# Performance work log

Hardware: AMD Instinct MI355X
Metric: run time of the kernel (lower is better)

## Reference

```python
import jax, jax.numpy as jnp
import numpy as np

B, H, D, DV, N, M = 1, 8, 64, 64, 2048, 128


def setup_inputs() -> dict:
    key = jax.random.key(0)
    k1, k2, k3, k4 = jax.random.split(key, 4)
    keys = jax.random.normal(k1, (B, H, D, N), dtype=jnp.float32)
    values = jax.random.normal(k2, (B, H, DV, N), dtype=jnp.float32)
    queries = jax.random.normal(k3, (B, H, D, N), dtype=jnp.float32)
    # orthonormal random features: QR of (m, key_dim) gaussian (reduced QR, m >= key_dim)
    raw = np.asarray(jax.random.normal(k4, (M, D), dtype=jnp.float32), dtype=np.float64)
    features = jnp.asarray(np.linalg.qr(raw)[0], dtype=jnp.float32)  # (M, D)
    return {"keys": keys, "values": values, "queries": queries, "features": features}


def reference(keys, values, queries, features):
    b, h, d, n = keys.shape
    dv = values.shape[2]
    m = features.shape[0]
    phi_scale = 1.0 / jnp.sqrt(jnp.asarray(m, keys.dtype))
    # flatten heads into batch, move locations to axis 1: (B*H, N, D)
    k = keys.reshape(b * h, d, n).transpose(0, 2, 1)
    v = values.reshape(b * h, dv, n).transpose(0, 2, 1)
    q = queries.reshape(b * h, d, n).transpose(0, 2, 1)

    def phi(x):  # (BH, N, D) -> (BH, N, M); f=[relu], h(x)=1.0
        return jax.nn.relu(jnp.einsum('bnd,md->bnm', x, features)) * phi_scale

    phi_k = phi(k)
    phi_q = phi(q)
    # causal linear attention: prefix sums of phi_k (x) v outer products
    kv = jnp.cumsum(phi_k[:, :, :, None] * v[:, :, None, :], axis=1)  # (BH, N, M, DV)
    out = jnp.einsum('bnm,bnmv->bnv', phi_q, kv)                      # (BH, N, DV)
    norm = jnp.einsum('bnm,bnm->bn', phi_q, jnp.cumsum(phi_k, axis=1))
    out = out / norm[:, :, None]
    out = out.transpose(0, 2, 1).reshape(b, h, dv, n)
    return out
```

## Files before the change

### kernel.cpp

```cpp
#include <hip/hip_runtime.h>


#define BH 8
#define D 64
#define DV 64
#define NSEQ 2048
#define M 128
#define CHK 64
#define NC (NSEQ / CHK)
#define PHI_SCALE 0.08838834764831845f

typedef unsigned int uint;
typedef unsigned short ushort;
typedef __attribute__((ext_vector_type(8))) short bf16x8;
typedef __attribute__((ext_vector_type(4))) float f32x4;
#define MFMA16(a, b, c) __builtin_amdgcn_mfma_f32_16x16x32_bf16((a), (b), (c), 0, 0, 0)

__device__ __forceinline__ short f2bf(float x) {
    uint u = __float_as_uint(x);
    u += 0x7fffu + ((u >> 16) & 1u);
    return (short)(u >> 16);
}
__device__ __forceinline__ float bf2f(short b) {
    return __uint_as_float(((uint)(ushort)b) << 16);
}

__global__ __launch_bounds__(256) void favor_p1(
    const float* __restrict__ keys, const float* __restrict__ values,
    const float* __restrict__ features, ushort* __restrict__ St,
    float* __restrict__ z)
{
    const int bh = blockIdx.x >> 5, c = blockIdx.x & 31, n0 = c * CHK;
    const int tid = threadIdx.x;
    const int lane = tid & 63, wid = tid >> 6, quad = lane >> 4, l16 = lane & 15;

    __shared__ ulong2 smv[2048];
    short* sF  = (short*)smv;
    short* sPK = (short*)smv + 8192;

    for (int i = tid; i < 8192; i += 256) sF[i] = f2bf(features[i]);
    __syncthreads();

    {
        const float* Kb = keys + bh * D * NSEQ + n0 + 16 * wid + l16;
        bf16x8 bK[2];
        for (int h = 0; h < 2; ++h)
            for (int j = 0; j < 8; ++j)
                bK[h][j] = f2bf(Kb[(32 * h + 8 * quad + j) * NSEQ]);
        for (int mt = 0; mt < 8; ++mt) {
            f32x4 acc = {0.f, 0.f, 0.f, 0.f};
            for (int h = 0; h < 2; ++h) {
                bf16x8 aF = *(const bf16x8*)(sF + (16 * mt + l16) * 64 + 32 * h + 8 * quad);
                acc = MFMA16(aF, bK[h], acc);
            }
            for (int r = 0; r < 4; ++r)
                sPK[(16 * mt + 4 * quad + r) * 64 + 16 * wid + l16] =
                    f2bf(fmaxf(acc[r], 0.f) * PHI_SCALE);
        }
    }
    __syncthreads();

    if (tid < 128) {
        float s = 0.f;
        for (int n = 0; n < 64; ++n) s += bf2f(sPK[tid * 64 + ((n + tid) & 63)]);
        z[(bh * NC + c) * M + tid] = s;
    }

    {
        const float* Vb = values + bh * DV * NSEQ + n0;
        bf16x8 aV[2];
        for (int h = 0; h < 2; ++h) {
            const float4* vp = (const float4*)(Vb + (16 * wid + l16) * NSEQ + 32 * h + 8 * quad);
            float4 v0 = vp[0], v1 = vp[1];
            aV[h][0] = f2bf(v0.x); aV[h][1] = f2bf(v0.y);
            aV[h][2] = f2bf(v0.z); aV[h][3] = f2bf(v0.w);
            aV[h][4] = f2bf(v1.x); aV[h][5] = f2bf(v1.y);
            aV[h][6] = f2bf(v1.z); aV[h][7] = f2bf(v1.w);
        }
        ushort* So = St + (size_t)(bh * NC + c) * (DV * M);
        for (int mt = 0; mt < 8; ++mt) {
            f32x4 acc = {0.f, 0.f, 0.f, 0.f};
            for (int h = 0; h < 2; ++h) {
                bf16x8 bP = *(const bf16x8*)(sPK + (16 * mt + l16) * 64 + 32 * h + 8 * quad);
                acc = MFMA16(aV[h], bP, acc);
            }
            for (int r = 0; r < 4; ++r)
                So[(16 * wid + 4 * quad + r) * M + 16 * mt + l16] = (ushort)f2bf(acc[r]);
        }
    }
}

__global__ __launch_bounds__(256) void favor_p2(ushort* __restrict__ St,
                                                float* __restrict__ z)
{
    const int gid = blockIdx.x * 256 + threadIdx.x;
    if (blockIdx.x < 256) {
        const int bh = gid >> 13, vm = gid & 8191;
        ushort* p = St + (size_t)bh * NC * 8192 + vm;
        float vals[NC];
        #pragma unroll
        for (int cc = 0; cc < NC; ++cc) vals[cc] = bf2f(p[cc * 8192]);
        float run = 0.f;
        #pragma unroll
        for (int cc = 0; cc < NC; ++cc) { p[cc * 8192] = (ushort)f2bf(run); run += vals[cc]; }
    } else {
        const int i = gid - 65536;
        if (i < BH * M) {
            const int bh = i >> 7, m = i & 127;
            float* p = z + bh * NC * M + m;
            float vals[NC];
            #pragma unroll
            for (int cc = 0; cc < NC; ++cc) vals[cc] = p[cc * M];
            float run = 0.f;
            #pragma unroll
            for (int cc = 0; cc < NC; ++cc) { p[cc * M] = run; run += vals[cc]; }
        }
    }
}

__global__ __launch_bounds__(256) void favor_p3(
    const float* __restrict__ keys, const float* __restrict__ values,
    const float* __restrict__ queries, const ushort* __restrict__ St,
    const float* __restrict__ z, const float* __restrict__ features,
    float* __restrict__ out)
{
    const int bh = blockIdx.x >> 5, c = blockIdx.x & 31, n0 = c * CHK;
    const int tid = threadIdx.x;
    const int lane = tid & 63, wid = tid >> 6, quad = lane >> 4, l16 = lane & 15;

    __shared__ ulong2 smv[3120];
    char* sm = (char*)smv;
    short* sF   = (short*)sm;
    short* sAm  = (short*)sm;
    short* sV   = (short*)(sm + 8192);
    short* sPQ  = (short*)(sm + 16384);
    float* sOut = (float*)(sm + 16384);
    short* sPK  = (short*)(sm + 32768);
    float* sZ   = (float*)(sm + 49152);
    float* sNm  = (float*)(sm + 49664);

    for (int i = tid; i < 8192; i += 256) sF[i] = f2bf(features[i]);
    if (tid < 128) sZ[tid] = z[(bh * NC + c) * M + tid];
    __syncthreads();

    {
        const float* Qb = queries + bh * D * NSEQ + n0 + 16 * wid + l16;
        const float* Kb = keys    + bh * D * NSEQ + n0 + 16 * wid + l16;
        bf16x8 aQ[2], aK[2];
        for (int h = 0; h < 2; ++h)
            for (int j = 0; j < 8; ++j) {
                const int d = 32 * h + 8 * quad + j;
                aQ[h][j] = f2bf(Qb[d * NSEQ]);
                aK[h][j] = f2bf(Kb[d * NSEQ]);
            }
        for (int mt = 0; mt < 8; ++mt) {
            f32x4 accQ = {0.f, 0.f, 0.f, 0.f}, accK = {0.f, 0.f, 0.f, 0.f};
            for (int h = 0; h < 2; ++h) {
                bf16x8 bF = *(const bf16x8*)(sF + (16 * mt + l16) * 64 + 32 * h + 8 * quad);
                accQ = MFMA16(aQ[h], bF, accQ);
                accK = MFMA16(aK[h], bF, accK);
            }
            for (int r = 0; r < 4; ++r) {
                const int row = (16 * wid + 4 * quad + r) * M + 16 * mt + l16;
                sPQ[row] = f2bf(fmaxf(accQ[r], 0.f) * PHI_SCALE);
                sPK[row] = f2bf(fmaxf(accK[r], 0.f) * PHI_SCALE);
            }
        }
    }
    __syncthreads();

    f32x4 accO[4], accC[4];
    for (int t = 0; t < 4; ++t) { accO[t] = (f32x4){0.f,0.f,0.f,0.f}; accC[t] = (f32x4){0.f,0.f,0.f,0.f}; }
    {
        const ushort* Sb = St + (size_t)(bh * NC + c) * (DV * M);
        for (int mt = 0; mt < 4; ++mt) {
            bf16x8 aP = *(const bf16x8*)(sPQ + (16 * wid + l16) * M + 32 * mt + 8 * quad);
            for (int vt = 0; vt < 4; ++vt) {
                bf16x8 bS = *(const bf16x8*)(Sb + (16 * vt + l16) * M + 32 * mt + 8 * quad);
                accO[vt] = MFMA16(aP, bS, accO[vt]);
            }
            for (int jt = 0; jt < 4; ++jt) {
                bf16x8 bK2 = *(const bf16x8*)(sPK + (16 * jt + l16) * M + 32 * mt + 8 * quad);
                accC[jt] = MFMA16(aP, bK2, accC[jt]);
            }
        }
    }
    float rsum[4] = {0.f, 0.f, 0.f, 0.f};
    for (int jt = 0; jt < 4; ++jt)
        for (int r = 0; r < 4; ++r) {
            const int n = 16 * wid + 4 * quad + r;
            const int j = 16 * jt + l16;
            const float av = (j <= n) ? accC[jt][r] : 0.f;
            rsum[r] += av;
            sAm[n * 64 + j] = f2bf(av);
        }
    for (int r = 0; r < 4; ++r) {
        float s = rsum[r];
        s += __shfl_xor(s, 1); s += __shfl_xor(s, 2);
        s += __shfl_xor(s, 4); s += __shfl_xor(s, 8);
        if (l16 == 0) sNm[16 * wid + 4 * quad + r] = s;
    }
    __syncthreads();

    for (int i = tid; i < 4096; i += 256) {
        const int v = i >> 6, j = i & 63;
        sV[v * 64 + j] = f2bf(values[(bh * DV + v) * NSEQ + n0 + j]);
    }
    if (tid < 64) {
        float s = 0.f;
        for (int mm = 0; mm < 128; ++mm) {
            const int m = (mm + 2 * tid) & 127;
            s += bf2f(sPQ[tid * M + m]) * sZ[m];
        }
        sNm[tid] += s;
    }
    __syncthreads();

    for (int jh = 0; jh < 2; ++jh) {
        bf16x8 aA = *(const bf16x8*)(sAm + (16 * wid + l16) * 64 + 32 * jh + 8 * quad);
        for (int vt = 0; vt < 4; ++vt) {
            bf16x8 bV = *(const bf16x8*)(sV + (16 * vt + l16) * 64 + 32 * jh + 8 * quad);
            accO[vt] = MFMA16(aA, bV, accO[vt]);
        }
    }
    for (int vt = 0; vt < 4; ++vt)
        for (int r = 0; r < 4; ++r) {
            const int n = 16 * wid + 4 * quad + r, v = 16 * vt + l16;
            sOut[n * 65 + v] = accO[vt][r] / sNm[n];
        }
    __syncthreads();

    for (int i = tid; i < 4096; i += 256) {
        const int v = i >> 6, n = i & 63;
        out[(bh * DV + v) * NSEQ + n0 + n] = sOut[n * 65 + v];
    }
}

extern "C" void kernel_launch(void* const* d_in, const int* in_sizes, int n_in,
                              void* d_out, int out_size, void* d_ws, size_t ws_size,
                              hipStream_t stream)
{
    (void)in_sizes; (void)n_in; (void)out_size; (void)ws_size;
    const float* keys     = (const float*)d_in[0];
    const float* values   = (const float*)d_in[1];
    const float* queries  = (const float*)d_in[2];
    const float* features = (const float*)d_in[3];
    float* outp = (float*)d_out;

    ushort* St = (ushort*)d_ws;
    float*  z  = (float*)((char*)d_ws + (size_t)BH * NC * DV * M * sizeof(ushort));

    favor_p1<<<dim3(BH * NC), dim3(256), 0, stream>>>(keys, values, features, St, z);
    favor_p2<<<dim3(260), dim3(256), 0, stream>>>(St, z);
    favor_p3<<<dim3(BH * NC), dim3(256), 0, stream>>>(keys, values, queries, St, z,
                                                      features, outp);
}
```

Baseline: 91.66 us.

## Restructure into four-kernel pipeline with pre-transposed bf16 inputs and smaller chunks

Adds a pre-pass kernel that converts queries, keys and features to bf16 in transposed, row-contiguous layouts. All intra-chunk work (phi_q, phi_k, chunk states, the causal intra-chunk output and its normalizer) moves into the first pass, so the final pass only applies the prefix state, adds the stored intra-chunk result and normalizes. Chunk size drops from 64 to 32, which doubles the number of blocks and halves per-block work to improve parallelism. In exchange it adds a kernel launch and extra workspace traffic for phiQ, Y and the normalizer, and doubles the state tensor and the length of the prefix scan.

```diff
diff --git a/kernel.cpp b/kernel.cpp
--- a/kernel.cpp
+++ b/kernel.cpp
@@ -2,12 +2,12 @@
 
 
 #define BH 8
-#define D 64
+#define DD 64
 #define DV 64
 #define NSEQ 2048
-#define M 128
-#define CHK 64
-#define NC (NSEQ / CHK)
+#define MM 128
+#define CK 32
+#define NCH (NSEQ / CK)
 #define PHI_SCALE 0.08838834764831845f
 
 typedef unsigned int uint;
@@ -21,73 +21,183 @@
     u += 0x7fffu + ((u >> 16) & 1u);
     return (short)(u >> 16);
 }
-__device__ __forceinline__ float bf2f(short b) {
-    return __uint_as_float(((uint)(ushort)b) << 16);
+__device__ __forceinline__ float bf2f(ushort b) {
+    return __uint_as_float(((uint)b) << 16);
+}
+
+#define OFF_QT   0u
+#define OFF_KT   2097152u
+#define OFF_FB   4194304u
+#define OFF_PQT  4210688u
+#define OFF_ST   8404992u
+#define OFF_Z    16793600u
+#define OFF_Y    17055744u
+#define OFF_NI   21250048u
+
+__global__ __launch_bounds__(256) void favor_p0(
+    const float* __restrict__ keys, const float* __restrict__ queries,
+    const float* __restrict__ features, ushort* __restrict__ Qt,
+    ushort* __restrict__ Kt, ushort* __restrict__ Fb)
+{
+    const int b = blockIdx.x, tid = threadIdx.x;
+    if (b == 256) {
+        uint* fo = (uint*)Fb;
+        const float2* fi = (const float2*)features;
+        for (int i = tid; i < 4096; i += 256) {
+            float2 f = fi[i];
+            fo[i] = (uint)(ushort)f2bf(f.x) | ((uint)(ushort)f2bf(f.y) << 16);
+        }
+        return;
+    }
+    const int bh = b >> 5, nc = b & 31, n0 = nc * 64;
+    __shared__ short sT[64 * 66];
+    for (int pass = 0; pass < 2; ++pass) {
+        const float* src = pass ? keys : queries;
+        ushort* dst = pass ? Kt : Qt;
+        for (int i = tid; i < 4096; i += 256) {
+            const int d = i >> 6, n = i & 63;
+            sT[d * 66 + n] = f2bf(src[(bh * 64 + d) * NSEQ + n0 + n]);
+        }
+        __syncthreads();
+        uint* dw = (uint*)dst;
+        for (int i = tid; i < 2048; i += 256) {
+            const int n = i >> 5, dp = i & 31;
+            const uint lo = (ushort)sT[(2 * dp) * 66 + n];
+            const uint hi = (ushort)sT[(2 * dp + 1) * 66 + n];
+            dw[(size_t)(bh * NSEQ + n0 + n) * 32 + dp] = lo | (hi << 16);
+        }
+        __syncthreads();
+    }
 }
 
 __global__ __launch_bounds__(256) void favor_p1(
-    const float* __restrict__ keys, const float* __restrict__ values,
-    const float* __restrict__ features, ushort* __restrict__ St,
-    float* __restrict__ z)
-{
-    const int bh = blockIdx.x >> 5, c = blockIdx.x & 31, n0 = c * CHK;
+    const float* __restrict__ values, const ushort* __restrict__ Qt,
+    const ushort* __restrict__ Kt, const ushort* __restrict__ Fb,
+    ushort* __restrict__ phiQT, ushort* __restrict__ St,
+    float* __restrict__ z, float* __restrict__ Yw, float* __restrict__ normI)
+{
+    const int bh = blockIdx.x >> 6, ck = blockIdx.x & 63, n0 = ck * CK;
     const int tid = threadIdx.x;
     const int lane = tid & 63, wid = tid >> 6, quad = lane >> 4, l16 = lane & 15;
 
-    __shared__ ulong2 smv[2048];
-    short* sF  = (short*)smv;
-    short* sPK = (short*)smv + 8192;
-
-    for (int i = tid; i < 8192; i += 256) sF[i] = f2bf(features[i]);
-    __syncthreads();
-
-    {
-        const float* Kb = keys + bh * D * NSEQ + n0 + 16 * wid + l16;
-        bf16x8 bK[2];
+    __shared__ __align__(16) short sPQT[32 * 136];
+    __shared__ __align__(16) short sPKT[32 * 136];
+    __shared__ __align__(16) short sPK[128 * 40];
+    __shared__ __align__(16) short sV[64 * 40];
+    __shared__ __align__(16) short sAm[32 * 40];
+    __shared__ float sNI[64];
+
+    for (int i = tid; i < 2048; i += 256) {
+        const int v = i >> 5, j = i & 31;
+        sV[v * 40 + j] = f2bf(values[(bh * DV + v) * NSEQ + n0 + j]);
+    }
+
+    {
+        const int nt = wid & 1, mg = wid >> 1;
+        const ushort* qrow = Qt + (size_t)(bh * NSEQ + n0 + 16 * nt + l16) * 64;
+        const ushort* krow = Kt + (size_t)(bh * NSEQ + n0 + 16 * nt + l16) * 64;
+        bf16x8 aQ[2], aK[2];
+        for (int h = 0; h < 2; ++h) {
+            aQ[h] = *(const bf16x8*)(qrow + 32 * h + 8 * quad);
+            aK[h] = *(const bf16x8*)(krow + 32 * h + 8 * quad);
+        }
+        for (int t = 0; t < 4; ++t) {
+            const int mt = mg * 4 + t;
+            f32x4 accQ = {0.f, 0.f, 0.f, 0.f}, accK = {0.f, 0.f, 0.f, 0.f};
+            for (int h = 0; h < 2; ++h) {
+                bf16x8 bF = *(const bf16x8*)(Fb + (16 * mt + l16) * 64 + 32 * h + 8 * quad);
+                accQ = MFMA16(aQ[h], bF, accQ);
+                accK = MFMA16(aK[h], bF, accK);
+            }
+            for (int r = 0; r < 4; ++r) {
+                const int nl = 16 * nt + 4 * quad + r, m = 16 * mt + l16;
+                sPQT[nl * 136 + m] = f2bf(fmaxf(accQ[r], 0.f) * PHI_SCALE);
+                sPKT[nl * 136 + m] = f2bf(fmaxf(accK[r], 0.f) * PHI_SCALE);
+            }
+        }
+    }
+    for (int t = 0; t < 2; ++t) {
+        const int mt = wid * 2 + t;
+        bf16x8 aF[2];
         for (int h = 0; h < 2; ++h)
-            for (int j = 0; j < 8; ++j)
-                bK[h][j] = f2bf(Kb[(32 * h + 8 * quad + j) * NSEQ]);
-        for (int mt = 0; mt < 8; ++mt) {
+            aF[h] = *(const bf16x8*)(Fb + (16 * mt + l16) * 64 + 32 * h + 8 * quad);
+        for (int ntt = 0; ntt < 2; ++ntt) {
             f32x4 acc = {0.f, 0.f, 0.f, 0.f};
             for (int h = 0; h < 2; ++h) {
-                bf16x8 aF = *(const bf16x8*)(sF + (16 * mt + l16) * 64 + 32 * h + 8 * quad);
-                acc = MFMA16(aF, bK[h], acc);
+                bf16x8 bK = *(const bf16x8*)(Kt + (size_t)(bh * NSEQ + n0 + 16 * ntt + l16) * 64 + 32 * h + 8 * quad);
+                acc = MFMA16(aF[h], bK, acc);
             }
             for (int r = 0; r < 4; ++r)
-                sPK[(16 * mt + 4 * quad + r) * 64 + 16 * wid + l16] =
+                sPK[(16 * mt + 4 * quad + r) * 40 + 16 * ntt + l16] =
                     f2bf(fmaxf(acc[r], 0.f) * PHI_SCALE);
         }
     }
     __syncthreads();
 
+    {
+        const int vt = wid;
+        bf16x8 aV = *(const bf16x8*)(sV + (16 * vt + l16) * 40 + 8 * quad);
+        ushort* So = St + (size_t)(bh * NCH + ck) * (DV * MM);
+        for (int mt = 0; mt < 8; ++mt) {
+            bf16x8 bP = *(const bf16x8*)(sPK + (16 * mt + l16) * 40 + 8 * quad);
+            f32x4 acc = {0.f, 0.f, 0.f, 0.f};
+            acc = MFMA16(aV, bP, acc);
+            for (int r = 0; r < 4; ++r)
+                So[(16 * vt + 4 * quad + r) * MM + 16 * mt + l16] = (ushort)f2bf(acc[r]);
+        }
+    }
     if (tid < 128) {
         float s = 0.f;
-        for (int n = 0; n < 64; ++n) s += bf2f(sPK[tid * 64 + ((n + tid) & 63)]);
-        z[(bh * NC + c) * M + tid] = s;
-    }
-
-    {
-        const float* Vb = values + bh * DV * NSEQ + n0;
-        bf16x8 aV[2];
-        for (int h = 0; h < 2; ++h) {
-            const float4* vp = (const float4*)(Vb + (16 * wid + l16) * NSEQ + 32 * h + 8 * quad);
-            float4 v0 = vp[0], v1 = vp[1];
-            aV[h][0] = f2bf(v0.x); aV[h][1] = f2bf(v0.y);
-            aV[h][2] = f2bf(v0.z); aV[h][3] = f2bf(v0.w);
-            aV[h][4] = f2bf(v1.x); aV[h][5] = f2bf(v1.y);
-            aV[h][6] = f2bf(v1.z); aV[h][7] = f2bf(v1.w);
-        }
-        ushort* So = St + (size_t)(bh * NC + c) * (DV * M);
-        for (int mt = 0; mt < 8; ++mt) {
+        for (int n = 0; n < 32; ++n) s += bf2f((ushort)sPKT[n * 136 + tid]);
+        z[(bh * NCH + ck) * MM + tid] = s;
+    }
+    {
+        const uint* sp = (const uint*)sPQT;
+        uint* pq = (uint*)(phiQT + (size_t)(bh * NSEQ + n0) * MM);
+        for (int i = tid; i < 2048; i += 256) {
+            const int n = i >> 6, mp = i & 63;
+            pq[n * 64 + mp] = sp[n * 68 + mp];
+        }
+    }
+    {
+        const int nt = wid & 1, jt = wid >> 1;
+        f32x4 acc = {0.f, 0.f, 0.f, 0.f};
+        for (int mc = 0; mc < 4; ++mc) {
+            bf16x8 aP = *(const bf16x8*)(sPQT + (16 * nt + l16) * 136 + 32 * mc + 8 * quad);
+            bf16x8 bP = *(const bf16x8*)(sPKT + (16 * jt + l16) * 136 + 32 * mc + 8 * quad);
+            acc = MFMA16(aP, bP, acc);
+        }
+        float rs[4];
+        for (int r = 0; r < 4; ++r) {
+            const int nl = 16 * nt + 4 * quad + r, jl = 16 * jt + l16;
+            const float av = (jl <= nl) ? acc[r] : 0.f;
+            rs[r] = av;
+            sAm[nl * 40 + jl] = f2bf(av);
+        }
+        for (int r = 0; r < 4; ++r) {
+            float s = rs[r];
+            s += __shfl_xor(s, 1); s += __shfl_xor(s, 2);
+            s += __shfl_xor(s, 4); s += __shfl_xor(s, 8);
+            if (l16 == 0) sNI[jt * 32 + 16 * nt + 4 * quad + r] = s;
+        }
+    }
+    __syncthreads();
+
+    {
+        const int nt = wid & 1, vb = (wid >> 1) * 2;
+        bf16x8 aA = *(const bf16x8*)(sAm + (16 * nt + l16) * 40 + 8 * quad);
+        for (int t = 0; t < 2; ++t) {
+            const int vt = vb + t;
+            bf16x8 bV = *(const bf16x8*)(sV + (16 * vt + l16) * 40 + 8 * quad);
             f32x4 acc = {0.f, 0.f, 0.f, 0.f};
-            for (int h = 0; h < 2; ++h) {
-                bf16x8 bP = *(const bf16x8*)(sPK + (16 * mt + l16) * 64 + 32 * h + 8 * quad);
-                acc = MFMA16(aV[h], bP, acc);
-            }
-            for (int r = 0; r < 4; ++r)
-                So[(16 * wid + 4 * quad + r) * M + 16 * mt + l16] = (ushort)f2bf(acc[r]);
-        }
-    }
+            acc = MFMA16(aA, bV, acc);
+            for (int r = 0; r < 4; ++r) {
+                const int nl = 16 * nt + 4 * quad + r, v = 16 * vt + l16;
+                Yw[(size_t)(bh * NSEQ + n0 + nl) * DV + v] = acc[r];
+            }
+        }
+    }
+    if (tid < 32) normI[bh * NSEQ + n0 + tid] = sNI[tid] + sNI[32 + tid];
 }
 
 __global__ __launch_bounds__(256) void favor_p2(ushort* __restrict__ St,
@@ -96,143 +206,102 @@
     const int gid = blockIdx.x * 256 + threadIdx.x;
     if (blockIdx.x < 256) {
         const int bh = gid >> 13, vm = gid & 8191;
-        ushort* p = St + (size_t)bh * NC * 8192 + vm;
-        float vals[NC];
-        #pragma unroll
-        for (int cc = 0; cc < NC; ++cc) vals[cc] = bf2f(p[cc * 8192]);
+        ushort* p = St + (size_t)bh * NCH * 8192 + vm;
         float run = 0.f;
-        #pragma unroll
-        for (int cc = 0; cc < NC; ++cc) { p[cc * 8192] = (ushort)f2bf(run); run += vals[cc]; }
+        for (int half = 0; half < 2; ++half) {
+            float vals[32];
+            #pragma unroll
+            for (int cc = 0; cc < 32; ++cc) vals[cc] = bf2f(p[(32 * half + cc) * 8192]);
+            #pragma unroll
+            for (int cc = 0; cc < 32; ++cc) {
+                p[(32 * half + cc) * 8192] = (ushort)f2bf(run);
+                run += vals[cc];
+            }
+        }
     } else {
         const int i = gid - 65536;
-        if (i < BH * M) {
+        if (i < BH * MM) {
             const int bh = i >> 7, m = i & 127;
-            float* p = z + bh * NC * M + m;
-            float vals[NC];
-            #pragma unroll
-            for (int cc = 0; cc < NC; ++cc) vals[cc] = p[cc * M];
+            float* p = z + bh * NCH * MM + m;
             float run = 0.f;
-            #pragma unroll
-            for (int cc = 0; cc < NC; ++cc) { p[cc * M] = run; run += vals[cc]; }
+            for (int half = 0; half < 2; ++half) {
+                float vals[32];
+                #pragma unroll
+                for (int cc = 0; cc < 32; ++cc) vals[cc] = p[(32 * half + cc) * MM];
+                #pragma unroll
+                for (int cc = 0; cc < 32; ++cc) {
+                    p[(32 * half + cc) * MM] = run;
+                    run += vals[cc];
+                }
+            }
         }
     }
 }
 
 __global__ __launch_bounds__(256) void favor_p3(
-    const float* __restrict__ keys, const float* __restrict__ values,
-    const float* __restrict__ queries, const ushort* __restrict__ St,
-    const float* __restrict__ z, const float* __restrict__ features,
-    float* __restrict__ out)
-{
-    const int bh = blockIdx.x >> 5, c = blockIdx.x & 31, n0 = c * CHK;
+    const ushort* __restrict__ phiQT, const ushort* __restrict__ St,
+    const float* __restrict__ z, const float* __restrict__ Yw,
+    const float* __restrict__ normI, float* __restrict__ out)
+{
+    const int bh = blockIdx.x >> 6, ck = blockIdx.x & 63, n0 = ck * CK;
     const int tid = threadIdx.x;
     const int lane = tid & 63, wid = tid >> 6, quad = lane >> 4, l16 = lane & 15;
 
-    __shared__ ulong2 smv[3120];
-    char* sm = (char*)smv;
-    short* sF   = (short*)sm;
-    short* sAm  = (short*)sm;
-    short* sV   = (short*)(sm + 8192);
-    short* sPQ  = (short*)(sm + 16384);
-    float* sOut = (float*)(sm + 16384);
-    short* sPK  = (short*)(sm + 32768);
-    float* sZ   = (float*)(sm + 49152);
-    float* sNm  = (float*)(sm + 49664);
-
-    for (int i = tid; i < 8192; i += 256) sF[i] = f2bf(features[i]);
-    if (tid < 128) sZ[tid] = z[(bh * NC + c) * M + tid];
-    __syncthreads();
-
-    {
-        const float* Qb = queries + bh * D * NSEQ + n0 + 16 * wid + l16;
-        const float* Kb = keys    + bh * D * NSEQ + n0 + 16 * wid + l16;
-        bf16x8 aQ[2], aK[2];
-        for (int h = 0; h < 2; ++h)
-            for (int j = 0; j < 8; ++j) {
-                const int d = 32 * h + 8 * quad + j;
-                aQ[h][j] = f2bf(Qb[d * NSEQ]);
-                aK[h][j] = f2bf(Kb[d * NSEQ]);
-            }
-        for (int mt = 0; mt < 8; ++mt) {
-            f32x4 accQ = {0.f, 0.f, 0.f, 0.f}, accK = {0.f, 0.f, 0.f, 0.f};
-            for (int h = 0; h < 2; ++h) {
-                bf16x8 bF = *(const bf16x8*)(sF + (16 * mt + l16) * 64 + 32 * h + 8 * quad);
-                accQ = MFMA16(aQ[h], bF, accQ);
-                accK = MFMA16(aK[h], bF, accK);
-            }
-            for (int r = 0; r < 4; ++r) {
-                const int row = (16 * wid + 4 * quad + r) * M + 16 * mt + l16;
-                sPQ[row] = f2bf(fmaxf(accQ[r], 0.f) * PHI_SCALE);
-                sPK[row] = f2bf(fmaxf(accK[r], 0.f) * PHI_SCALE);
-            }
-        }
-    }
-    __syncthreads();
-
-    f32x4 accO[4], accC[4];
-    for (int t = 0; t < 4; ++t) { accO[t] = (f32x4){0.f,0.f,0.f,0.f}; accC[t] = (f32x4){0.f,0.f,0.f,0.f}; }
-    {
-        const ushort* Sb = St + (size_t)(bh * NC + c) * (DV * M);
-        for (int mt = 0; mt < 4; ++mt) {
-            bf16x8 aP = *(const bf16x8*)(sPQ + (16 * wid + l16) * M + 32 * mt + 8 * quad);
-            for (int vt = 0; vt < 4; ++vt) {
-                bf16x8 bS = *(const bf16x8*)(Sb + (16 * vt + l16) * M + 32 * mt + 8 * quad);
-                accO[vt] = MFMA16(aP, bS, accO[vt]);
-            }
-            for (int jt = 0; jt < 4; ++jt) {
-                bf16x8 bK2 = *(const bf16x8*)(sPK + (16 * jt + l16) * M + 32 * mt + 8 * quad);
-                accC[jt] = MFMA16(aP, bK2, accC[jt]);
-            }
-        }
-    }
-    float rsum[4] = {0.f, 0.f, 0.f, 0.f};
-    for (int jt = 0; jt < 4; ++jt)
+    __shared__ float sOut[32 * 66];
+    __shared__ float sPart[32 * 8];
+    __shared__ float sNm[32];
+
+    const ushort* pqt = phiQT + (size_t)(bh * NSEQ + n0) * MM;
+    const ushort* sb  = St + (size_t)(bh * NCH + ck) * 8192;
+
+    const int nt = wid & 1, vb = (wid >> 1) * 2;
+    bf16x8 aP[4];
+    for (int mc = 0; mc < 4; ++mc)
+        aP[mc] = *(const bf16x8*)(pqt + (16 * nt + l16) * MM + 32 * mc + 8 * quad);
+    f32x4 acc[2];
+    for (int t = 0; t < 2; ++t) {
+        acc[t] = (f32x4){0.f, 0.f, 0.f, 0.f};
+        const int vt = vb + t;
+        for (int mc = 0; mc < 4; ++mc) {
+            bf16x8 bS = *(const bf16x8*)(sb + (16 * vt + l16) * MM + 32 * mc + 8 * quad);
+            acc[t] = MFMA16(aP[mc], bS, acc[t]);
+        }
+    }
+
+    {
+        const int n = tid >> 3, seg = tid & 7;
+        const uint* pr = (const uint*)(pqt + n * MM + seg * 16);
+        const float* zz = z + (bh * NCH + ck) * MM + seg * 16;
+        float s = 0.f;
+        #pragma unroll
+        for (int k = 0; k < 8; ++k) {
+            const uint u = pr[k];
+            s += bf2f((ushort)(u & 0xffffu)) * zz[2 * k];
+            s += bf2f((ushort)(u >> 16)) * zz[2 * k + 1];
+        }
+        sPart[n * 8 + seg] = s;
+    }
+    __syncthreads();
+    if (tid < 32) {
+        float nm = normI[bh * NSEQ + n0 + tid];
+        #pragma unroll
+        for (int s8 = 0; s8 < 8; ++s8) nm += sPart[tid * 8 + s8];
+        sNm[tid] = nm;
+    }
+    __syncthreads();
+
+    for (int t = 0; t < 2; ++t) {
+        const int vt = vb + t;
         for (int r = 0; r < 4; ++r) {
-            const int n = 16 * wid + 4 * quad + r;
-            const int j = 16 * jt + l16;
-            const float av = (j <= n) ? accC[jt][r] : 0.f;
-            rsum[r] += av;
-            sAm[n * 64 + j] = f2bf(av);
-        }
-    for (int r = 0; r < 4; ++r) {
-        float s = rsum[r];
-        s += __shfl_xor(s, 1); s += __shfl_xor(s, 2);
-        s += __shfl_xor(s, 4); s += __shfl_xor(s, 8);
-        if (l16 == 0) sNm[16 * wid + 4 * quad + r] = s;
-    }
-    __syncthreads();
-
-    for (int i = tid; i < 4096; i += 256) {
-        const int v = i >> 6, j = i & 63;
-        sV[v * 64 + j] = f2bf(values[(bh * DV + v) * NSEQ + n0 + j]);
-    }
-    if (tid < 64) {
-        float s = 0.f;
-        for (int mm = 0; mm < 128; ++mm) {
-            const int m = (mm + 2 * tid) & 127;
-            s += bf2f(sPQ[tid * M + m]) * sZ[m];
-        }
-        sNm[tid] += s;
-    }
-    __syncthreads();
-
-    for (int jh = 0; jh < 2; ++jh) {
-        bf16x8 aA = *(const bf16x8*)(sAm + (16 * wid + l16) * 64 + 32 * jh + 8 * quad);
-        for (int vt = 0; vt < 4; ++vt) {
-            bf16x8 bV = *(const bf16x8*)(sV + (16 * vt + l16) * 64 + 32 * jh + 8 * quad);
-            accO[vt] = MFMA16(aA, bV, accO[vt]);
-        }
-    }
-    for (int vt = 0; vt < 4; ++vt)
-        for (int r = 0; r < 4; ++r) {
-            const int n = 16 * wid + 4 * quad + r, v = 16 * vt + l16;
-            sOut[n * 65 + v] = accO[vt][r] / sNm[n];
-        }
-    __syncthreads();
-
-    for (int i = tid; i < 4096; i += 256) {
-        const int v = i >> 6, n = i & 63;
-        out[(bh * DV + v) * NSEQ + n0 + n] = sOut[n * 65 + v];
+            const int nl = 16 * nt + 4 * quad + r, v = 16 * vt + l16;
+            const float y = Yw[(size_t)(bh * NSEQ + n0 + nl) * DV + v];
+            sOut[nl * 66 + v] = (acc[t][r] + y) / sNm[nl];
+        }
+    }
+    __syncthreads();
+    for (int i = tid; i < 2048; i += 256) {
+        const int v = i >> 5, n = i & 31;
+        out[(bh * DV + v) * NSEQ + n0 + n] = sOut[n * 66 + v];
     }
 }
 
@@ -247,11 +316,18 @@
     const float* features = (const float*)d_in[3];
     float* outp = (float*)d_out;
 
-    ushort* St = (ushort*)d_ws;
-    float*  z  = (float*)((char*)d_ws + (size_t)BH * NC * DV * M * sizeof(ushort));
-
-    favor_p1<<<dim3(BH * NC), dim3(256), 0, stream>>>(keys, values, features, St, z);
+    char* ws = (char*)d_ws;
+    ushort* Qt    = (ushort*)(ws + OFF_QT);
+    ushort* Kt    = (ushort*)(ws + OFF_KT);
+    ushort* Fb    = (ushort*)(ws + OFF_FB);
+    ushort* phiQT = (ushort*)(ws + OFF_PQT);
+    ushort* St    = (ushort*)(ws + OFF_ST);
+    float*  z     = (float*)(ws + OFF_Z);
+    float*  Yw    = (float*)(ws + OFF_Y);
+    float*  nI    = (float*)(ws + OFF_NI);
+
+    favor_p0<<<dim3(257), dim3(256), 0, stream>>>(keys, queries, features, Qt, Kt, Fb);
+    favor_p1<<<dim3(512), dim3(256), 0, stream>>>(values, Qt, Kt, Fb, phiQT, St, z, Yw, nI);
     favor_p2<<<dim3(260), dim3(256), 0, stream>>>(St, z);
-    favor_p3<<<dim3(BH * NC), dim3(256), 0, stream>>>(keys, values, queries, St, z,
-                                                      features, outp);
-}
+    favor_p3<<<dim3(512), dim3(256), 0, stream>>>(phiQT, St, z, Yw, nI, outp);
+}
```

Measured after the change: 98.12 us. +7.0%, slower.

## Fuse three phases into one persistent kernel with grid barriers and smaller chunks

Applied to the files above, without the earlier changes.

Replaces the three-kernel pipeline (chunk state, prefix scan, output) with one init kernel that converts features to bf16 and clears barrier counters, plus a single 256-block main kernel. The main kernel computes phi once, syncs all blocks through atomic grid barriers for the cross-chunk prefix scan, then finishes the output. Chunks shrink to 32 tokens, each block handling two. This removes the recomputation of phi_k/phi_q, the duplicate loads and the launch gaps, but depends on all 256 blocks being co-resident for the spin barrier. It adds a doubled 64-deep scan and serialized barrier latency.

```diff
diff --git a/kernel.cpp b/kernel.cpp
--- a/kernel.cpp
+++ b/kernel.cpp
@@ -2,12 +2,13 @@
 
 
 #define BH 8
-#define D 64
+#define DD 64
 #define DV 64
 #define NSEQ 2048
-#define M 128
-#define CHK 64
-#define NC (NSEQ / CHK)
+#define MM 128
+#define CK 32
+#define NCH 64
+#define NBLK 256
 #define PHI_SCALE 0.08838834764831845f
 
 typedef unsigned int uint;
@@ -21,218 +22,242 @@
     u += 0x7fffu + ((u >> 16) & 1u);
     return (short)(u >> 16);
 }
-__device__ __forceinline__ float bf2f(short b) {
-    return __uint_as_float(((uint)(ushort)b) << 16);
-}
-
-__global__ __launch_bounds__(256) void favor_p1(
+__device__ __forceinline__ float bf2f(ushort b) {
+    return __uint_as_float(((uint)b) << 16);
+}
+
+#define OFF_Z   8388608u
+#define OFF_FB  8650752u
+#define OFF_BAR 8667136u
+
+__global__ __launch_bounds__(256) void favor_init(
+    const float* __restrict__ features, ushort* __restrict__ Fb,
+    uint* __restrict__ bar)
+{
+    const int tid = threadIdx.x;
+    if (tid < 32) bar[tid] = 0u;
+    uint* fo = (uint*)Fb;
+    const float2* fi = (const float2*)features;
+    for (int i = tid; i < 4096; i += 256) {
+        float2 f = fi[i];
+        fo[i] = (uint)(ushort)f2bf(f.x) | ((uint)(ushort)f2bf(f.y) << 16);
+    }
+}
+
+__device__ __forceinline__ void gbar(uint* cnt)
+{
+    __syncthreads();
+    if (threadIdx.x == 0) {
+        __threadfence();
+        __hip_atomic_fetch_add(cnt, 1u, __ATOMIC_ACQ_REL, __HIP_MEMORY_SCOPE_AGENT);
+        while (__hip_atomic_load(cnt, __ATOMIC_ACQUIRE, __HIP_MEMORY_SCOPE_AGENT) < NBLK) {}
+        __threadfence();
+    }
+    __syncthreads();
+}
+
+__global__ __launch_bounds__(256, 2) void favor_main(
     const float* __restrict__ keys, const float* __restrict__ values,
-    const float* __restrict__ features, ushort* __restrict__ St,
-    float* __restrict__ z)
-{
-    const int bh = blockIdx.x >> 5, c = blockIdx.x & 31, n0 = c * CHK;
+    const float* __restrict__ queries, const ushort* __restrict__ Fb,
+    ushort* __restrict__ St, float* __restrict__ z, uint* __restrict__ bar,
+    float* __restrict__ out)
+{
+    const int b = blockIdx.x;
+    const int bh = b >> 5, pr_ = b & 31;
     const int tid = threadIdx.x;
     const int lane = tid & 63, wid = tid >> 6, quad = lane >> 4, l16 = lane & 15;
-
-    __shared__ ulong2 smv[2048];
-    short* sF  = (short*)smv;
-    short* sPK = (short*)smv + 8192;
-
-    for (int i = tid; i < 8192; i += 256) sF[i] = f2bf(features[i]);
-    __syncthreads();
-
-    {
-        const float* Kb = keys + bh * D * NSEQ + n0 + 16 * wid + l16;
-        bf16x8 bK[2];
-        for (int h = 0; h < 2; ++h)
-            for (int j = 0; j < 8; ++j)
-                bK[h][j] = f2bf(Kb[(32 * h + 8 * quad + j) * NSEQ]);
-        for (int mt = 0; mt < 8; ++mt) {
-            f32x4 acc = {0.f, 0.f, 0.f, 0.f};
-            for (int h = 0; h < 2; ++h) {
-                bf16x8 aF = *(const bf16x8*)(sF + (16 * mt + l16) * 64 + 32 * h + 8 * quad);
-                acc = MFMA16(aF, bK[h], acc);
-            }
-            for (int r = 0; r < 4; ++r)
-                sPK[(16 * mt + 4 * quad + r) * 64 + 16 * wid + l16] =
-                    f2bf(fmaxf(acc[r], 0.f) * PHI_SCALE);
-        }
-    }
-    __syncthreads();
-
-    if (tid < 128) {
-        float s = 0.f;
-        for (int n = 0; n < 64; ++n) s += bf2f(sPK[tid * 64 + ((n + tid) & 63)]);
-        z[(bh * NC + c) * M + tid] = s;
-    }
-
-    {
-        const float* Vb = values + bh * DV * NSEQ + n0;
-        bf16x8 aV[2];
-        for (int h = 0; h < 2; ++h) {
-            const float4* vp = (const float4*)(Vb + (16 * wid + l16) * NSEQ + 32 * h + 8 * quad);
-            float4 v0 = vp[0], v1 = vp[1];
-            aV[h][0] = f2bf(v0.x); aV[h][1] = f2bf(v0.y);
-            aV[h][2] = f2bf(v0.z); aV[h][3] = f2bf(v0.w);
-            aV[h][4] = f2bf(v1.x); aV[h][5] = f2bf(v1.y);
-            aV[h][6] = f2bf(v1.z); aV[h][7] = f2bf(v1.w);
-        }
-        ushort* So = St + (size_t)(bh * NC + c) * (DV * M);
-        for (int mt = 0; mt < 8; ++mt) {
-            f32x4 acc = {0.f, 0.f, 0.f, 0.f};
-            for (int h = 0; h < 2; ++h) {
-                bf16x8 bP = *(const bf16x8*)(sPK + (16 * mt + l16) * 64 + 32 * h + 8 * quad);
-                acc = MFMA16(aV[h], bP, acc);
-            }
-            for (int r = 0; r < 4; ++r)
-                So[(16 * wid + 4 * quad + r) * M + 16 * mt + l16] = (ushort)f2bf(acc[r]);
-        }
-    }
-}
-
-__global__ __launch_bounds__(256) void favor_p2(ushort* __restrict__ St,
-                                                float* __restrict__ z)
-{
-    const int gid = blockIdx.x * 256 + threadIdx.x;
-    if (blockIdx.x < 256) {
-        const int bh = gid >> 13, vm = gid & 8191;
-        ushort* p = St + (size_t)bh * NC * 8192 + vm;
-        float vals[NC];
-        #pragma unroll
-        for (int cc = 0; cc < NC; ++cc) vals[cc] = bf2f(p[cc * 8192]);
-        float run = 0.f;
-        #pragma unroll
-        for (int cc = 0; cc < NC; ++cc) { p[cc * 8192] = (ushort)f2bf(run); run += vals[cc]; }
-    } else {
-        const int i = gid - 65536;
-        if (i < BH * M) {
-            const int bh = i >> 7, m = i & 127;
-            float* p = z + bh * NC * M + m;
-            float vals[NC];
-            #pragma unroll
-            for (int cc = 0; cc < NC; ++cc) vals[cc] = p[cc * M];
-            float run = 0.f;
-            #pragma unroll
-            for (int cc = 0; cc < NC; ++cc) { p[cc * M] = run; run += vals[cc]; }
-        }
-    }
-}
-
-__global__ __launch_bounds__(256) void favor_p3(
-    const float* __restrict__ keys, const float* __restrict__ values,
-    const float* __restrict__ queries, const ushort* __restrict__ St,
-    const float* __restrict__ z, const float* __restrict__ features,
-    float* __restrict__ out)
-{
-    const int bh = blockIdx.x >> 5, c = blockIdx.x & 31, n0 = c * CHK;
-    const int tid = threadIdx.x;
-    const int lane = tid & 63, wid = tid >> 6, quad = lane >> 4, l16 = lane & 15;
-
-    __shared__ ulong2 smv[3120];
-    char* sm = (char*)smv;
-    short* sF   = (short*)sm;
-    short* sAm  = (short*)sm;
-    short* sV   = (short*)(sm + 8192);
-    short* sPQ  = (short*)(sm + 16384);
-    float* sOut = (float*)(sm + 16384);
-    short* sPK  = (short*)(sm + 32768);
-    float* sZ   = (float*)(sm + 49152);
-    float* sNm  = (float*)(sm + 49664);
-
-    for (int i = tid; i < 8192; i += 256) sF[i] = f2bf(features[i]);
-    if (tid < 128) sZ[tid] = z[(bh * NC + c) * M + tid];
-    __syncthreads();
-
-    {
-        const float* Qb = queries + bh * D * NSEQ + n0 + 16 * wid + l16;
-        const float* Kb = keys    + bh * D * NSEQ + n0 + 16 * wid + l16;
+    const int ch = wid >> 1, sw = wid & 1;
+    const int ck = 2 * pr_ + ch, n0c = ck * CK;
+
+    __shared__ __align__(16) char sm[60672];
+    short* sPQT = (short*)sm;
+    short* sPKT = (short*)(sm + 17408);
+    short* sPK  = (short*)(sm + 34816);
+    short* sAm  = (short*)(sm + 55296);
+    float* sNI  = (float*)(sm + 60416);
+    float* sOut = (float*)(sm + 17408);
+    float* sPart= (float*)(sm + 34816);
+    float* sNm  = (float*)(sm + 36352);
+
+    short* pqt = sPQT + ch * 4352;
+    short* pkt = sPKT + ch * 4352;
+    short* ppk = sPK + ch * 5120;
+
+    for (int i = tid; i < 1280; i += 256) ((uint*)sAm)[i] = 0u;
+
+    {
+        const float* Qb = queries + (size_t)(bh * DD) * NSEQ + n0c + 16 * sw + l16;
+        const float* Kb = keys    + (size_t)(bh * DD) * NSEQ + n0c + 16 * sw + l16;
         bf16x8 aQ[2], aK[2];
         for (int h = 0; h < 2; ++h)
             for (int j = 0; j < 8; ++j) {
                 const int d = 32 * h + 8 * quad + j;
-                aQ[h][j] = f2bf(Qb[d * NSEQ]);
-                aK[h][j] = f2bf(Kb[d * NSEQ]);
+                aQ[h][j] = f2bf(Qb[(size_t)d * NSEQ]);
+                aK[h][j] = f2bf(Kb[(size_t)d * NSEQ]);
             }
         for (int mt = 0; mt < 8; ++mt) {
             f32x4 accQ = {0.f, 0.f, 0.f, 0.f}, accK = {0.f, 0.f, 0.f, 0.f};
             for (int h = 0; h < 2; ++h) {
-                bf16x8 bF = *(const bf16x8*)(sF + (16 * mt + l16) * 64 + 32 * h + 8 * quad);
+                bf16x8 bF = *(const bf16x8*)(Fb + (16 * mt + l16) * 64 + 32 * h + 8 * quad);
                 accQ = MFMA16(aQ[h], bF, accQ);
                 accK = MFMA16(aK[h], bF, accK);
             }
             for (int r = 0; r < 4; ++r) {
-                const int row = (16 * wid + 4 * quad + r) * M + 16 * mt + l16;
-                sPQ[row] = f2bf(fmaxf(accQ[r], 0.f) * PHI_SCALE);
-                sPK[row] = f2bf(fmaxf(accK[r], 0.f) * PHI_SCALE);
-            }
-        }
-    }
-    __syncthreads();
-
-    f32x4 accO[4], accC[4];
-    for (int t = 0; t < 4; ++t) { accO[t] = (f32x4){0.f,0.f,0.f,0.f}; accC[t] = (f32x4){0.f,0.f,0.f,0.f}; }
-    {
-        const ushort* Sb = St + (size_t)(bh * NC + c) * (DV * M);
-        for (int mt = 0; mt < 4; ++mt) {
-            bf16x8 aP = *(const bf16x8*)(sPQ + (16 * wid + l16) * M + 32 * mt + 8 * quad);
-            for (int vt = 0; vt < 4; ++vt) {
-                bf16x8 bS = *(const bf16x8*)(Sb + (16 * vt + l16) * M + 32 * mt + 8 * quad);
-                accO[vt] = MFMA16(aP, bS, accO[vt]);
-            }
-            for (int jt = 0; jt < 4; ++jt) {
-                bf16x8 bK2 = *(const bf16x8*)(sPK + (16 * jt + l16) * M + 32 * mt + 8 * quad);
-                accC[jt] = MFMA16(aP, bK2, accC[jt]);
-            }
-        }
-    }
-    float rsum[4] = {0.f, 0.f, 0.f, 0.f};
-    for (int jt = 0; jt < 4; ++jt)
+                const int nl = 16 * sw + 4 * quad + r, m = 16 * mt + l16;
+                pqt[nl * 136 + m] = f2bf(fmaxf(accQ[r], 0.f) * PHI_SCALE);
+                const short pk = f2bf(fmaxf(accK[r], 0.f) * PHI_SCALE);
+                pkt[nl * 136 + m] = pk;
+                ppk[m * 40 + nl] = pk;
+            }
+        }
+    }
+    __syncthreads();
+
+    {
+        const int zch = tid >> 7, m = tid & 127;
+        const short* pp = sPK + zch * 5120 + m * 40;
+        float s = 0.f;
+        for (int n = 0; n < CK; ++n) s += bf2f((ushort)pp[(n + m) & 31]);
+        z[(size_t)(bh * NCH + 2 * pr_ + zch) * MM + m] = s;
+    }
+
+    {
+        ushort* So = St + (size_t)(bh * NCH + ck) * (DV * MM);
+        const float* Vb = values + (size_t)(bh * DV) * NSEQ + n0c;
+        for (int t = 0; t < 2; ++t) {
+            const int vt = 2 * sw + t;
+            const float4* vp = (const float4*)(Vb + (size_t)(16 * vt + l16) * NSEQ + 8 * quad);
+            float4 v0 = vp[0], v1 = vp[1];
+            bf16x8 aV;
+            aV[0] = f2bf(v0.x); aV[1] = f2bf(v0.y); aV[2] = f2bf(v0.z); aV[3] = f2bf(v0.w);
+            aV[4] = f2bf(v1.x); aV[5] = f2bf(v1.y); aV[6] = f2bf(v1.z); aV[7] = f2bf(v1.w);
+            for (int mt = 0; mt < 8; ++mt) {
+                bf16x8 bP = *(const bf16x8*)(ppk + (16 * mt + l16) * 40 + 8 * quad);
+                f32x4 acc = {0.f, 0.f, 0.f, 0.f};
+                acc = MFMA16(aV, bP, acc);
+                for (int r = 0; r < 4; ++r)
+                    So[(16 * vt + 4 * quad + r) * MM + 16 * mt + l16] = (ushort)f2bf(acc[r]);
+            }
+        }
+    }
+
+    {
+        float rs[4] = {0.f, 0.f, 0.f, 0.f};
+        for (int jt = 0; jt <= sw; ++jt) {
+            f32x4 acc = {0.f, 0.f, 0.f, 0.f};
+            for (int mc = 0; mc < 4; ++mc) {
+                bf16x8 aP = *(const bf16x8*)(pqt + (16 * sw + l16) * 136 + 32 * mc + 8 * quad);
+                bf16x8 bP = *(const bf16x8*)(pkt + (16 * jt + l16) * 136 + 32 * mc + 8 * quad);
+                acc = MFMA16(aP, bP, acc);
+            }
+            for (int r = 0; r < 4; ++r) {
+                const int nl = 16 * sw + 4 * quad + r, jl = 16 * jt + l16;
+                const float av = (jl <= nl) ? acc[r] : 0.f;
+                rs[r] += av;
+                sAm[ch * 1280 + nl * 40 + jl] = f2bf(av);
+            }
+        }
         for (int r = 0; r < 4; ++r) {
-            const int n = 16 * wid + 4 * quad + r;
-            const int j = 16 * jt + l16;
-            const float av = (j <= n) ? accC[jt][r] : 0.f;
-            rsum[r] += av;
-            sAm[n * 64 + j] = f2bf(av);
-        }
-    for (int r = 0; r < 4; ++r) {
-        float s = rsum[r];
-        s += __shfl_xor(s, 1); s += __shfl_xor(s, 2);
-        s += __shfl_xor(s, 4); s += __shfl_xor(s, 8);
-        if (l16 == 0) sNm[16 * wid + 4 * quad + r] = s;
-    }
-    __syncthreads();
-
-    for (int i = tid; i < 4096; i += 256) {
-        const int v = i >> 6, j = i & 63;
-        sV[v * 64 + j] = f2bf(values[(bh * DV + v) * NSEQ + n0 + j]);
-    }
+            float s = rs[r];
+            s += __shfl_xor(s, 1); s += __shfl_xor(s, 2);
+            s += __shfl_xor(s, 4); s += __shfl_xor(s, 8);
+            if (l16 == 0) sNI[ch * 32 + 16 * sw + 4 * quad + r] = s;
+        }
+    }
+
+    f32x4 acc[4];
+    {
+        bf16x8 aA = *(const bf16x8*)(sAm + ch * 1280 + (16 * sw + l16) * 40 + 8 * quad);
+        const float* Vb = values + (size_t)(bh * DV) * NSEQ + n0c;
+        for (int vt = 0; vt < 4; ++vt) {
+            const float4* vp = (const float4*)(Vb + (size_t)(16 * vt + l16) * NSEQ + 8 * quad);
+            float4 v0 = vp[0], v1 = vp[1];
+            bf16x8 bV;
+            bV[0] = f2bf(v0.x); bV[1] = f2bf(v0.y); bV[2] = f2bf(v0.z); bV[3] = f2bf(v0.w);
+            bV[4] = f2bf(v1.x); bV[5] = f2bf(v1.y); bV[6] = f2bf(v1.z); bV[7] = f2bf(v1.w);
+            acc[vt] = (f32x4){0.f, 0.f, 0.f, 0.f};
+            acc[vt] = MFMA16(aA, bV, acc[vt]);
+        }
+    }
+
+    gbar(bar + 0);
+    {
+        const int gid = b * 256 + tid;
+        const int sbh = gid >> 13, vm = gid & 8191;
+        ushort* p = St + (size_t)sbh * (NCH * 8192) + vm;
+        float run = 0.f;
+        for (int half = 0; half < 2; ++half) {
+            float vals[32];
+            #pragma unroll
+            for (int cc = 0; cc < 32; ++cc) vals[cc] = bf2f(p[(size_t)(32 * half + cc) * 8192]);
+            #pragma unroll
+            for (int cc = 0; cc < 32; ++cc) {
+                p[(size_t)(32 * half + cc) * 8192] = (ushort)f2bf(run);
+                run += vals[cc];
+            }
+        }
+        if (b < 4) {
+            const int zc = b * 256 + tid;
+            const int zbh = zc >> 7, m = zc & 127;
+            float* pz = z + (size_t)zbh * (NCH * MM) + m;
+            float zr = 0.f;
+            for (int half = 0; half < 2; ++half) {
+                float zv[32];
+                #pragma unroll
+                for (int cc = 0; cc < 32; ++cc) zv[cc] = pz[(32 * half + cc) * MM];
+                #pragma unroll
+                for (int cc = 0; cc < 32; ++cc) {
+                    pz[(32 * half + cc) * MM] = zr;
+                    zr += zv[cc];
+                }
+            }
+        }
+    }
+    gbar(bar + 1);
+
+    {
+        const ushort* sb = St + (size_t)(bh * NCH + ck) * 8192;
+        bf16x8 aP[4];
+        for (int mc = 0; mc < 4; ++mc)
+            aP[mc] = *(const bf16x8*)(pqt + (16 * sw + l16) * 136 + 32 * mc + 8 * quad);
+        for (int vt = 0; vt < 4; ++vt)
+            for (int mc = 0; mc < 4; ++mc) {
+                bf16x8 bS = *(const bf16x8*)(sb + (16 * vt + l16) * MM + 32 * mc + 8 * quad);
+                acc[vt] = MFMA16(aP[mc], bS, acc[vt]);
+            }
+    }
+    {
+        const int nch = tid >> 7, t2 = tid & 127, n = t2 >> 2, seg = t2 & 3;
+        const uint* pr2 = (const uint*)(sPQT + nch * 4352) + n * 68 + seg * 16;
+        const float* zz = z + (size_t)(bh * NCH + 2 * pr_ + nch) * MM + seg * 32;
+        float s = 0.f;
+        #pragma unroll
+        for (int k = 0; k < 16; ++k) {
+            const uint u = pr2[k];
+            s += bf2f((ushort)(u & 0xffffu)) * zz[2 * k];
+            s += bf2f((ushort)(u >> 16)) * zz[2 * k + 1];
+        }
+        sPart[nch * 128 + n * 4 + seg] = s;
+    }
+    __syncthreads();
     if (tid < 64) {
-        float s = 0.f;
-        for (int mm = 0; mm < 128; ++mm) {
-            const int m = (mm + 2 * tid) & 127;
-            s += bf2f(sPQ[tid * M + m]) * sZ[m];
-        }
-        sNm[tid] += s;
-    }
-    __syncthreads();
-
-    for (int jh = 0; jh < 2; ++jh) {
-        bf16x8 aA = *(const bf16x8*)(sAm + (16 * wid + l16) * 64 + 32 * jh + 8 * quad);
-        for (int vt = 0; vt < 4; ++vt) {
-            bf16x8 bV = *(const bf16x8*)(sV + (16 * vt + l16) * 64 + 32 * jh + 8 * quad);
-            accO[vt] = MFMA16(aA, bV, accO[vt]);
-        }
-    }
+        const int nch = tid >> 5, n = tid & 31;
+        float nm = sNI[nch * 32 + n];
+        #pragma unroll
+        for (int s4 = 0; s4 < 4; ++s4) nm += sPart[nch * 128 + n * 4 + s4];
+        sNm[nch * 32 + n] = nm;
+    }
+    __syncthreads();
     for (int vt = 0; vt < 4; ++vt)
         for (int r = 0; r < 4; ++r) {
-            const int n = 16 * wid + 4 * quad + r, v = 16 * vt + l16;
-            sOut[n * 65 + v] = accO[vt][r] / sNm[n];
-        }
-    __syncthreads();
-
+            const int nl = 16 * sw + 4 * quad + r, v = 16 * vt + l16;
+            sOut[ch * 2112 + nl * 66 + v] = acc[vt][r] / sNm[ch * 32 + nl];
+        }
+    __syncthreads();
     for (int i = tid; i < 4096; i += 256) {
-        const int v = i >> 6, n = i & 63;
-        out[(bh * DV + v) * NSEQ + n0 + n] = sOut[n * 65 + v];
+        const int och = i >> 11, rem = i & 2047, v = rem >> 5, n = rem & 31;
+        out[(size_t)(bh * DV + v) * NSEQ + (2 * pr_ + och) * CK + n] =
+            sOut[och * 2112 + n * 66 + v];
     }
 }
 
@@ -247,11 +272,13 @@
     const float* features = (const float*)d_in[3];
     float* outp = (float*)d_out;
 
-    ushort* St = (ushort*)d_ws;
-    float*  z  = (float*)((char*)d_ws + (size_t)BH * NC * DV * M * sizeof(ushort));
-
-    favor_p1<<<dim3(BH * NC), dim3(256), 0, stream>>>(keys, values, features, St, z);
-    favor_p2<<<dim3(260), dim3(256), 0, stream>>>(St, z);
-    favor_p3<<<dim3(BH * NC), dim3(256), 0, stream>>>(keys, values, queries, St, z,
-                                                      features, outp);
-}
+    char* ws = (char*)d_ws;
+    ushort* St = (ushort*)ws;
+    float*  z  = (float*)(ws + OFF_Z);
+    ushort* Fb = (ushort*)(ws + OFF_FB);
+    uint*   bar = (uint*)(ws + OFF_BAR);
+
+    favor_init<<<dim3(1), dim3(256), 0, stream>>>(features, Fb, bar);
+    favor_main<<<dim3(NBLK), dim3(256), 0, stream>>>(keys, values, queries, Fb,
+                                                     St, z, bar, outp);
+}
```

Measured after the change: 146.7 us. +60.0%, slower.
